# Performance work log

Measured on AMD Instinct MI355X. Metric: run time of the kernel, lower is better.

## Reference

```python
import jax, jax.numpy as jnp
import numpy as np

# Grid config from init_kwargs
VX, VY = 0.1, 0.1
XMIN, YMIN, ZMIN, XMAX, YMAX, ZMAX = 0.0, -25.6, -3.0, 51.2, 25.6, 3.0
H = int(round((XMAX - XMIN) / VX))  # 512
W = int(round((YMAX - YMIN) / VY))  # 512
SIGMA = 1.5   # gaussian std in voxel units
R = 3         # splat window radius -> 7x7 kernel


def _pose0to1(pose0, pose1):
    # ego-motion: pose1^{-1} @ pose0, per batch element
    return jnp.linalg.inv(pose1) @ pose0


def _transform(xyz, pose):
    # xyz: [B,N,3], pose: [B,4,4] -> xyz @ R^T + t
    Rm = pose[:, :3, :3]
    t = pose[:, :3, 3]
    return jnp.einsum('bnd,bed->bne', xyz, Rm) + t[:, None, :]


def _voxelize(xyz):
    # continuous voxel coords + integer pillar indices + in-range mask
    px = (xyz[..., 0] - XMIN) / VX
    py = (xyz[..., 1] - YMIN) / VY
    ix = jnp.floor(px).astype(jnp.int32)
    iy = jnp.floor(py).astype(jnp.int32)
    valid = (ix >= 0) & (ix < H) & (iy >= 0) & (iy < W) & \
            (xyz[..., 2] >= ZMIN) & (xyz[..., 2] < ZMAX)
    return px, py, ix, iy, valid


def _gauss_heatmap(px, py, ix, iy, valid):
    # Splat a gaussian (max-composited) around every valid radar pillar.
    B, M = px.shape
    offs = jnp.arange(-R, R + 1)
    dx, dy = jnp.meshgrid(offs, offs, indexing='ij')      # [K,K]
    gx = ix[:, :, None, None] + dx                        # [B,M,K,K]
    gy = iy[:, :, None, None] + dy
    cellx = gx.astype(px.dtype) + 0.5
    celly = gy.astype(py.dtype) + 0.5
    d2 = (cellx - px[:, :, None, None]) ** 2 + (celly - py[:, :, None, None]) ** 2
    val = jnp.exp(-d2 / (2.0 * SIGMA * SIGMA))
    inb = (gx >= 0) & (gx < H) & (gy >= 0) & (gy < W) & valid[:, :, None, None]
    bidx = jnp.arange(B, dtype=jnp.int32)[:, None, None, None]
    flat = jnp.where(inb, bidx * (H * W) + gx * W + gy, B * H * W)  # dummy seg for invalid
    heat = jax.ops.segment_max(val.reshape(-1), flat.reshape(-1),
                               num_segments=B * H * W + 1)
    heat = jnp.maximum(heat[:B * H * W], 0.0).reshape(B, H, W)
    return heat


def _gather(heat, ix, iy, valid):
    # per-point gaussian score = heatmap at the point's pillar
    B = heat.shape[0]
    hf = heat.reshape(B, -1)
    idx = jnp.clip(ix, 0, H - 1) * W + jnp.clip(iy, 0, W - 1)
    s = jnp.take_along_axis(hf, idx, axis=1)
    return jnp.where(valid, s, 0.0)


def _forward(pc0, pc1, radar_pc0, radar_pc1, pose0, pose1):
    # pose computed under no_grad in the original -> stop_gradient
    pose_0to1 = jax.lax.stop_gradient(_pose0to1(pose0, pose1))
    tpc0 = _transform(pc0, pose_0to1)
    trad0_xyz = _transform(radar_pc0[..., :3], pose_0to1)
    # dynamic pillar voxelization (BEV coords)
    _, _, l0x, l0y, l0v = _voxelize(tpc0)
    _, _, l1x, l1y, l1v = _voxelize(pc1)
    r0px, r0py, r0x, r0y, r0v = _voxelize(trad0_xyz)
    r1px, r1py, r1x, r1y, r1v = _voxelize(radar_pc1[..., :3])
    # gaussian maps from radar pillars, scored for lidar + radar points
    heat0 = _gauss_heatmap(r0px, r0py, r0x, r0y, r0v)
    heat1 = _gauss_heatmap(r1px, r1py, r1x, r1y, r1v)
    lidar0 = _gather(heat0, l0x, l0y, l0v)   # [B,N]
    radar0 = _gather(heat0, r0x, r0y, r0v)   # [B,M]
    lidar1 = _gather(heat1, l1x, l1y, l1v)
    radar1 = _gather(heat1, r1x, r1y, r1v)
    return jnp.concatenate([lidar0, radar0, lidar1, radar1], axis=1)


def setup_inputs() -> dict:
    key = jax.random.key(0)
    ks = jax.random.split(key, 8)
    B, N, M = 8, 262144, 8192
    lo = jnp.array([XMIN, YMIN, ZMIN], dtype=jnp.float32)
    hi = jnp.array([XMAX, YMAX, ZMAX], dtype=jnp.float32)
    pc0 = jax.random.uniform(ks[0], (B, N, 3), dtype=jnp.float32) * (hi - lo) + lo
    pc1 = jax.random.uniform(ks[1], (B, N, 3), dtype=jnp.float32) * (hi - lo) + lo
    rxyz0 = jax.random.uniform(ks[2], (B, M, 3), dtype=jnp.float32) * (hi - lo) + lo
    rxyz1 = jax.random.uniform(ks[3], (B, M, 3), dtype=jnp.float32) * (hi - lo) + lo
    radar_pc0 = jnp.concatenate([rxyz0, jax.random.normal(ks[4], (B, M, 3), dtype=jnp.float32)], axis=-1)
    radar_pc1 = jnp.concatenate([rxyz1, jax.random.normal(ks[5], (B, M, 3), dtype=jnp.float32)], axis=-1)

    def mk_pose(k):
        t = jax.random.uniform(k, (B, 3), minval=-0.5, maxval=0.5, dtype=jnp.float32)
        eye = jnp.tile(jnp.eye(4, dtype=jnp.float32)[None], (B, 1, 1))
        return eye.at[:, :3, 3].set(t)

    pose0 = mk_pose(ks[6])
    pose1 = mk_pose(ks[7])
    return {"pc0": pc0, "pc1": pc1, "radar_pc0": radar_pc0,
            "radar_pc1": radar_pc1, "pose0": pose0, "pose1": pose1}


def reference(pc0, pc1, radar_pc0, radar_pc1, pose0, pose1):
    return _forward(pc0, pc1, radar_pc0, radar_pc1, pose0, pose1)
```

## Files before the change

kernel.cpp:

```cpp
#include <hip/hip_runtime.h>
#include <math.h>

#define GH 512
#define GW 512
#define GHW (GH * GW)
#define RR 3
#define SH 16
#define SSHIFT 4
#define NSTRIP (GH / SH)
#define SCAP 1024
#define THR 1024
#define GTHR 256

typedef float f32x4 __attribute__((ext_vector_type(4)));


__device__ __forceinline__ void compute_pose(const float* __restrict__ P0,
                                             const float* __restrict__ P1,
                                             float* __restrict__ T) {
    float a00 = P1[0], a01 = P1[1], a02 = P1[2],  t1x = P1[3];
    float a10 = P1[4], a11 = P1[5], a12 = P1[6],  t1y = P1[7];
    float a20 = P1[8], a21 = P1[9], a22 = P1[10], t1z = P1[11];
    float c00 = a11 * a22 - a12 * a21;
    float c01 = a12 * a20 - a10 * a22;
    float c02 = a10 * a21 - a11 * a20;
    float det = a00 * c00 + a01 * c01 + a02 * c02;
    float id = 1.0f / det;
    float r00 = c00 * id;
    float r01 = (a02 * a21 - a01 * a22) * id;
    float r02 = (a01 * a12 - a02 * a11) * id;
    float r10 = c01 * id;
    float r11 = (a00 * a22 - a02 * a20) * id;
    float r12 = (a02 * a10 - a00 * a12) * id;
    float r20 = c02 * id;
    float r21 = (a01 * a20 - a00 * a21) * id;
    float r22 = (a00 * a11 - a01 * a10) * id;

    float b00 = P0[0], b01 = P0[1], b02 = P0[2],  t0x = P0[3];
    float b10 = P0[4], b11 = P0[5], b12 = P0[6],  t0y = P0[7];
    float b20 = P0[8], b21 = P0[9], b22 = P0[10], t0z = P0[11];
    float dx = t0x - t1x, dy = t0y - t1y, dz = t0z - t1z;

    T[0]  = r00 * b00 + r01 * b10 + r02 * b20;
    T[1]  = r00 * b01 + r01 * b11 + r02 * b21;
    T[2]  = r00 * b02 + r01 * b12 + r02 * b22;
    T[3]  = r00 * dx + r01 * dy + r02 * dz;
    T[4]  = r10 * b00 + r11 * b10 + r12 * b20;
    T[5]  = r10 * b01 + r11 * b11 + r12 * b21;
    T[6]  = r10 * b02 + r11 * b12 + r12 * b22;
    T[7]  = r10 * dx + r11 * dy + r12 * dz;
    T[8]  = r20 * b00 + r21 * b10 + r22 * b20;
    T[9]  = r20 * b01 + r21 * b11 + r22 * b21;
    T[10] = r20 * b02 + r21 * b12 + r22 * b22;
    T[11] = r20 * dx + r21 * dy + r22 * dz;
}

__device__ __forceinline__ void voxelize_xyz(float x, float y, float z,
                                             const float* __restrict__ T,
                                             float& px, float& py,
                                             int& ix, int& iy, bool& valid) {
    if (T) {
        float nx = T[0] * x + T[1] * y + T[2] * z + T[3];
        float ny = T[4] * x + T[5] * y + T[6] * z + T[7];
        float nz = T[8] * x + T[9] * y + T[10] * z + T[11];
        x = nx; y = ny; z = nz;
    }
    px = (x - 0.0f) * 10.0f;
    py = (y - (-25.6f)) * 10.0f;
    ix = (int)floorf(px);
    iy = (int)floorf(py);
    valid = (ix >= 0) & (ix < GH) & (iy >= 0) & (iy < GW) &
            (z >= -3.0f) & (z < 3.0f);
}

__global__ __launch_bounds__(THR, 8)
void heat_strip_kernel(const float* __restrict__ radar0,
                       const float* __restrict__ radar1,
                       const float* __restrict__ pose0,
                       const float* __restrict__ pose1,
                       float* __restrict__ heat0,
                       float* __restrict__ heat1,
                       int B, int M) {
    __shared__ int strip[SH * GW];
    __shared__ float2 sp[SCAP];
    __shared__ float Tsh[8][12];
    __shared__ int sn;

    const int tid = threadIdx.x;
    const int lane = tid & 63;
    const int blk = blockIdx.x;
    const int b = blk % B;
    const int map = (blk / B) & 1;
    const int sx = blk / (2 * B);
    const int x0 = sx << SSHIFT;

    if (tid < B) compute_pose(pose0 + tid * 16, pose1 + tid * 16, &Tsh[tid][0]);
    if (tid == 0) sn = 0;
    {
        const int4 z4 = make_int4(0, 0, 0, 0);
        for (int c4 = tid * 4; c4 < SH * GW; c4 += 4 * THR)
            *reinterpret_cast<int4*>(&strip[c4]) = z4;
    }
    __syncthreads();

    const float* radar = map ? radar1 : radar0;
    const float* pb = radar + (size_t)b * M * 6;
    const f32x4* pb4 = reinterpret_cast<const f32x4*>(pb);
    const bool hasT = (map == 0);
    const float* T = &Tsh[b][0];

    const int ng = M >> 2;
    for (int g0 = 0; g0 < ng; g0 += THR) {
        int g = g0 + tid;
        bool inr = (g < ng);
        float X[4], Y[4], Z[4];
        if (inr) {
            const f32x4* s = pb4 + (size_t)g * 6;
            f32x4 q0 = s[0], q1 = s[1], q2 = s[2];
            f32x4 q3 = s[3], q4 = s[4], q5 = s[5];
            X[0] = q0.x; Y[0] = q0.y; Z[0] = q0.z;
            X[1] = q1.z; Y[1] = q1.w; Z[1] = q2.x;
            X[2] = q3.x; Y[2] = q3.y; Z[2] = q3.z;
            X[3] = q4.z; Y[3] = q4.w; Z[3] = q5.x;
        }
        #pragma unroll
        for (int j = 0; j < 4; j++) {
            bool valid = false;
            float px = 0.0f, py = 0.0f;
            if (inr) {
                float x = X[j], y = Y[j], z = Z[j];
                float nx = hasT ? (T[0] * x + T[1] * y + T[2] * z + T[3]) : x;
                px = (nx - 0.0f) * 10.0f;
                int ix = (int)floorf(px);
                if (ix >= x0 - RR && ix <= x0 + SH - 1 + RR) {
                    float ny = hasT ? (T[4] * x + T[5] * y + T[6] * z + T[7]) : y;
                    float nz = hasT ? (T[8] * x + T[9] * y + T[10] * z + T[11]) : z;
                    py = (ny - (-25.6f)) * 10.0f;
                    int iy = (int)floorf(py);
                    valid = (ix >= 0) & (ix < GH) & (iy >= 0) & (iy < GW) &
                            (nz >= -3.0f) & (nz < 3.0f);
                }
            }
            unsigned long long mask = __ballot(valid);
            if (valid) {
                int leader = __ffsll((long long)mask) - 1;
                int cnt = __popcll(mask);
                int wbase = 0;
                if (lane == leader) wbase = atomicAdd(&sn, cnt);
                wbase = __shfl(wbase, leader);
                int off = __popcll(mask & ((1ull << lane) - 1ull));
                int slot = wbase + off;
                if (slot < SCAP) sp[slot] = make_float2(px, py);
            }
        }
    }
    if (M & 3) {
        int i = (M & ~3) + tid;
        bool valid = false;
        float px = 0.0f, py = 0.0f;
        if (i < M) {
            const float* p = pb + (size_t)i * 6;
            float x = p[0], y = p[1], z = p[2];
            float nx = hasT ? (T[0] * x + T[1] * y + T[2] * z + T[3]) : x;
            px = (nx - 0.0f) * 10.0f;
            int ix = (int)floorf(px);
            if (ix >= x0 - RR && ix <= x0 + SH - 1 + RR) {
                float ny = hasT ? (T[4] * x + T[5] * y + T[6] * z + T[7]) : y;
                float nz = hasT ? (T[8] * x + T[9] * y + T[10] * z + T[11]) : z;
                py = (ny - (-25.6f)) * 10.0f;
                int iy = (int)floorf(py);
                valid = (ix >= 0) & (ix < GH) & (iy >= 0) & (iy < GW) &
                        (nz >= -3.0f) & (nz < 3.0f);
            }
        }
        unsigned long long mask = __ballot(valid);
        if (valid) {
            int leader = __ffsll((long long)mask) - 1;
            int cnt = __popcll(mask);
            int wbase = 0;
            if (lane == leader) wbase = atomicAdd(&sn, cnt);
            wbase = __shfl(wbase, leader);
            int off = __popcll(mask & ((1ull << lane) - 1ull));
            int slot = wbase + off;
            if (slot < SCAP) sp[slot] = make_float2(px, py);
        }
    }
    __syncthreads();

    int n = sn; if (n > SCAP) n = SCAP;
    const int total = n * 49;
    for (int t = tid; t < total; t += THR) {
        int pi = t / 49;
        int c = t - pi * 49;
        float px = sp[pi].x;
        float py = sp[pi].y;
        int ix = (int)floorf(px);
        int iy = (int)floorf(py);
        int dx = c / 7 - RR;
        int dy = c - (c / 7) * 7 - RR;
        int gx = ix + dx, gy = iy + dy;
        if (gx < x0 || gx >= x0 + SH || gy < 0 || gy >= GW) continue;
        float ddx = ((float)gx + 0.5f) - px;
        float ddy = ((float)gy + 0.5f) - py;
        float d2 = ddx * ddx + ddy * ddy;
        float val = expf(-d2 / 4.5f);
        atomicMax(&strip[(gx - x0) * GW + gy], __float_as_int(val));
    }
    __syncthreads();

    float* heat = map ? heat1 : heat0;
    float* hb = heat + (size_t)b * GHW + (size_t)x0 * GW;
    for (int c4 = tid * 4; c4 < SH * GW; c4 += 4 * THR) {
        int4 iv = *reinterpret_cast<const int4*>(&strip[c4]);
        float4 fv;
        fv.x = __int_as_float(iv.x);
        fv.y = __int_as_float(iv.y);
        fv.z = __int_as_float(iv.z);
        fv.w = __int_as_float(iv.w);
        *reinterpret_cast<float4*>(hb + c4) = fv;
    }
}

__global__ __launch_bounds__(GTHR)
void gather_vec_kernel(const float* __restrict__ pc0,
                       const float* __restrict__ pc1,
                       const float* __restrict__ radar0,
                       const float* __restrict__ radar1,
                       const float* __restrict__ pose0,
                       const float* __restrict__ pose1,
                       const float* __restrict__ heat0,
                       const float* __restrict__ heat1,
                       float* __restrict__ out,
                       int N, int M) {
    __shared__ float Tsh[12];
    const int row_len = 2 * N + 2 * M;
    const int b = blockIdx.x;

    if (threadIdx.x == 0) compute_pose(pose0 + b * 16, pose1 + b * 16, Tsh);
    __syncthreads();

    const float* hb0 = heat0 + (size_t)b * GHW;
    const float* hb1 = heat1 + (size_t)b * GHW;

    const int ncp = N >> 10;
    const int ncr = M >> 10;
    const int c = blockIdx.y;

    const float* segbase;
    const float* T = nullptr;
    const float* hb;
    int stride, out_base, pseg;
    if (c < ncp) {
        segbase = pc0 + (size_t)b * N * 3; stride = 3;
        out_base = 0;          T = Tsh; hb = hb0; pseg = c << 10;
    } else if (c < ncp + ncr) {
        segbase = radar0 + (size_t)b * M * 6; stride = 6;
        out_base = N;          T = Tsh; hb = hb0; pseg = (c - ncp) << 10;
    } else if (c < 2 * ncp + ncr) {
        segbase = pc1 + (size_t)b * N * 3; stride = 3;
        out_base = N + M;               hb = hb1; pseg = (c - ncp - ncr) << 10;
    } else {
        segbase = radar1 + (size_t)b * M * 6; stride = 6;
        out_base = 2 * N + M;           hb = hb1; pseg = (c - 2 * ncp - ncr) << 10;
    }

    const int p0 = pseg + threadIdx.x * 4;
    float X[4], Y[4], Z[4];
    if (stride == 3) {
        const f32x4* s = reinterpret_cast<const f32x4*>(segbase + (size_t)p0 * 3);
        f32x4 f0 = __builtin_nontemporal_load(s + 0);
        f32x4 f1 = __builtin_nontemporal_load(s + 1);
        f32x4 f2 = __builtin_nontemporal_load(s + 2);
        X[0] = f0.x; Y[0] = f0.y; Z[0] = f0.z;
        X[1] = f0.w; Y[1] = f1.x; Z[1] = f1.y;
        X[2] = f1.z; Y[2] = f1.w; Z[2] = f2.x;
        X[3] = f2.y; Y[3] = f2.z; Z[3] = f2.w;
    } else {
        const f32x4* s = reinterpret_cast<const f32x4*>(segbase + (size_t)p0 * 6);
        f32x4 g0 = __builtin_nontemporal_load(s + 0);
        f32x4 g1 = __builtin_nontemporal_load(s + 1);
        f32x4 g2 = __builtin_nontemporal_load(s + 2);
        f32x4 g3 = __builtin_nontemporal_load(s + 3);
        f32x4 g4 = __builtin_nontemporal_load(s + 4);
        f32x4 g5 = __builtin_nontemporal_load(s + 5);
        X[0] = g0.x; Y[0] = g0.y; Z[0] = g0.z;
        X[1] = g1.z; Y[1] = g1.w; Z[1] = g2.x;
        X[2] = g3.x; Y[2] = g3.y; Z[2] = g3.z;
        X[3] = g4.z; Y[3] = g4.w; Z[3] = g5.x;
    }

    float v[4];
    #pragma unroll
    for (int k = 0; k < 4; k++) {
        float px, py; int ix, iy; bool valid;
        voxelize_xyz(X[k], Y[k], Z[k], T, px, py, ix, iy, valid);
        v[k] = 0.0f;
        if (valid) v[k] = hb[ix * GW + iy];
    }

    f32x4 res;
    res.x = v[0]; res.y = v[1]; res.z = v[2]; res.w = v[3];
    __builtin_nontemporal_store(res,
        reinterpret_cast<f32x4*>(out + (size_t)b * row_len + out_base + p0));
}

__global__ __launch_bounds__(GTHR)
void gather_fused_kernel(const float* __restrict__ pc0,
                         const float* __restrict__ pc1,
                         const float* __restrict__ radar0,
                         const float* __restrict__ radar1,
                         const float* __restrict__ pose0,
                         const float* __restrict__ pose1,
                         const float* __restrict__ heat0,
                         const float* __restrict__ heat1,
                         float* __restrict__ out,
                         int N, int M) {
    __shared__ float Tsh[12];
    const int row_len = 2 * N + 2 * M;
    const int b = blockIdx.x;
    const int base = blockIdx.y * 1024 + threadIdx.x;

    if (threadIdx.x == 0) compute_pose(pose0 + b * 16, pose1 + b * 16, Tsh);
    __syncthreads();

    const float* hb0 = heat0 + (size_t)b * GHW;
    const float* hb1 = heat1 + (size_t)b * GHW;

    #pragma unroll
    for (int k = 0; k < 4; k++) {
        int r = base + k * GTHR;
        if (r >= row_len) continue;
        const float* p;
        const float* T = nullptr;
        const float* hb;
        if (r < N) {
            p = pc0 + ((size_t)b * N + r) * 3; T = Tsh; hb = hb0;
        } else if (r < N + M) {
            p = radar0 + ((size_t)b * M + (r - N)) * 6; T = Tsh; hb = hb0;
        } else if (r < 2 * N + M) {
            p = pc1 + ((size_t)b * N + (r - N - M)) * 3; hb = hb1;
        } else {
            p = radar1 + ((size_t)b * M + (r - 2 * N - M)) * 6; hb = hb1;
        }
        float px, py; int ix, iy; bool valid;
        voxelize_xyz(p[0], p[1], p[2], T, px, py, ix, iy, valid);
        float v = 0.0f;
        if (valid) v = hb[ix * GW + iy];
        __builtin_nontemporal_store(v, out + (size_t)b * row_len + r);
    }
}

extern "C" void kernel_launch(void* const* d_in, const int* in_sizes, int n_in,
                              void* d_out, int out_size, void* d_ws, size_t ws_size,
                              hipStream_t stream) {
    const float* pc0      = (const float*)d_in[0];
    const float* pc1      = (const float*)d_in[1];
    const float* radar0   = (const float*)d_in[2];
    const float* radar1   = (const float*)d_in[3];
    const float* pose0    = (const float*)d_in[4];
    const float* pose1    = (const float*)d_in[5];
    float* out = (float*)d_out;

    int B = in_sizes[4] / 16;
    int N = in_sizes[0] / (B * 3);
    int M = in_sizes[2] / (B * 6);
    int row_len = 2 * N + 2 * M;

    float* heat0 = (float*)d_ws;
    float* heat1 = heat0 + (size_t)B * GHW;

    int nblk = 2 * B * NSTRIP;
    heat_strip_kernel<<<nblk, THR, 0, stream>>>(
        radar0, radar1, pose0, pose1, heat0, heat1, B, M);

    if (((N & 1023) == 0) && ((M & 1023) == 0)) {
        dim3 ggrid(B, 2 * (N >> 10) + 2 * (M >> 10));
        gather_vec_kernel<<<ggrid, GTHR, 0, stream>>>(
            pc0, pc1, radar0, radar1, pose0, pose1, heat0, heat1, out, N, M);
    } else {
        dim3 ggrid(B, (row_len + 1023) / 1024);
        gather_fused_kernel<<<ggrid, GTHR, 0, stream>>>(
            pc0, pc1, radar0, radar1, pose0, pose1, heat0, heat1, out, N, M);
    }
}
```

Baseline: 148.3 us.

## Stage gather inputs through LDS and double heat strip height

The gather kernel now copies each 1024-point chunk of the xyz input into shared memory with fully coalesced vector loads. Each thread then processes points at a stride of one block width, so the scalar output stores and heatmap reads are coalesced across lanes. Radar rows are read whole, including the unused 3 channels, which the old per-thread load also did. Separately, the heat strip height goes from 16 to 32 rows (halving the strip block count and doubling the strip LDS buffer) and the occupancy hint is dropped from the launch bounds.

After: 140.0 us. -5.6%, faster.

```diff
diff --git a/kernel.cpp b/kernel.cpp
--- a/kernel.cpp
+++ b/kernel.cpp
@@ -5,12 +5,13 @@
 #define GW 512
 #define GHW (GH * GW)
 #define RR 3
-#define SH 16
-#define SSHIFT 4
+#define SH 32
+#define SSHIFT 5
 #define NSTRIP (GH / SH)
 #define SCAP 1024
 #define THR 1024
 #define GTHR 256
+#define GCH 1024
 
 typedef float f32x4 __attribute__((ext_vector_type(4)));
 
@@ -73,7 +74,7 @@
             (z >= -3.0f) & (z < 3.0f);
 }
 
-__global__ __launch_bounds__(THR, 8)
+__global__ __launch_bounds__(THR)
 void heat_strip_kernel(const float* __restrict__ radar0,
                        const float* __restrict__ radar1,
                        const float* __restrict__ pose0,
@@ -222,7 +223,7 @@
 }
 
 __global__ __launch_bounds__(GTHR)
-void gather_vec_kernel(const float* __restrict__ pc0,
+void gather_lds_kernel(const float* __restrict__ pc0,
                        const float* __restrict__ pc1,
                        const float* __restrict__ radar0,
                        const float* __restrict__ radar1,
@@ -232,18 +233,16 @@
                        const float* __restrict__ heat1,
                        float* __restrict__ out,
                        int N, int M) {
+    __shared__ float stage[6 * GCH];
     __shared__ float Tsh[12];
+    const int tid = threadIdx.x;
     const int row_len = 2 * N + 2 * M;
     const int b = blockIdx.x;
 
-    if (threadIdx.x == 0) compute_pose(pose0 + b * 16, pose1 + b * 16, Tsh);
-    __syncthreads();
-
-    const float* hb0 = heat0 + (size_t)b * GHW;
-    const float* hb1 = heat1 + (size_t)b * GHW;
-
-    const int ncp = N >> 10;
-    const int ncr = M >> 10;
+    if (tid == 0) compute_pose(pose0 + b * 16, pose1 + b * 16, Tsh);
+
+    const int ncp = N / GCH;
+    const int ncr = M / GCH;
     const int c = blockIdx.y;
 
     const float* segbase;
@@ -252,56 +251,40 @@
     int stride, out_base, pseg;
     if (c < ncp) {
         segbase = pc0 + (size_t)b * N * 3; stride = 3;
-        out_base = 0;          T = Tsh; hb = hb0; pseg = c << 10;
+        out_base = 0;          T = Tsh; hb = heat0; pseg = c * GCH;
     } else if (c < ncp + ncr) {
         segbase = radar0 + (size_t)b * M * 6; stride = 6;
-        out_base = N;          T = Tsh; hb = hb0; pseg = (c - ncp) << 10;
+        out_base = N;          T = Tsh; hb = heat0; pseg = (c - ncp) * GCH;
     } else if (c < 2 * ncp + ncr) {
         segbase = pc1 + (size_t)b * N * 3; stride = 3;
-        out_base = N + M;               hb = hb1; pseg = (c - ncp - ncr) << 10;
+        out_base = N + M;               hb = heat1; pseg = (c - ncp - ncr) * GCH;
     } else {
         segbase = radar1 + (size_t)b * M * 6; stride = 6;
-        out_base = 2 * N + M;           hb = hb1; pseg = (c - 2 * ncp - ncr) << 10;
-    }
-
-    const int p0 = pseg + threadIdx.x * 4;
-    float X[4], Y[4], Z[4];
-    if (stride == 3) {
-        const f32x4* s = reinterpret_cast<const f32x4*>(segbase + (size_t)p0 * 3);
-        f32x4 f0 = __builtin_nontemporal_load(s + 0);
-        f32x4 f1 = __builtin_nontemporal_load(s + 1);
-        f32x4 f2 = __builtin_nontemporal_load(s + 2);
-        X[0] = f0.x; Y[0] = f0.y; Z[0] = f0.z;
-        X[1] = f0.w; Y[1] = f1.x; Z[1] = f1.y;
-        X[2] = f1.z; Y[2] = f1.w; Z[2] = f2.x;
-        X[3] = f2.y; Y[3] = f2.z; Z[3] = f2.w;
-    } else {
-        const f32x4* s = reinterpret_cast<const f32x4*>(segbase + (size_t)p0 * 6);
-        f32x4 g0 = __builtin_nontemporal_load(s + 0);
-        f32x4 g1 = __builtin_nontemporal_load(s + 1);
-        f32x4 g2 = __builtin_nontemporal_load(s + 2);
-        f32x4 g3 = __builtin_nontemporal_load(s + 3);
-        f32x4 g4 = __builtin_nontemporal_load(s + 4);
-        f32x4 g5 = __builtin_nontemporal_load(s + 5);
-        X[0] = g0.x; Y[0] = g0.y; Z[0] = g0.z;
-        X[1] = g1.z; Y[1] = g1.w; Z[1] = g2.x;
-        X[2] = g3.x; Y[2] = g3.y; Z[2] = g3.z;
-        X[3] = g4.z; Y[3] = g4.w; Z[3] = g5.x;
-    }
-
-    float v[4];
+        out_base = 2 * N + M;           hb = heat1; pseg = (c - 2 * ncp - ncr) * GCH;
+    }
+    const float* hbb = hb + (size_t)b * GHW;
+
+    {
+        const f32x4* src = reinterpret_cast<const f32x4*>(
+            segbase + (size_t)pseg * stride);
+        f32x4* dst = reinterpret_cast<f32x4*>(stage);
+        const int nv = (GCH * stride) >> 2;
+        for (int i = tid; i < nv; i += GTHR)
+            dst[i] = __builtin_nontemporal_load(src + i);
+    }
+    __syncthreads();
+
+    float* ob = out + (size_t)b * row_len + out_base + pseg;
     #pragma unroll
-    for (int k = 0; k < 4; k++) {
+    for (int j = 0; j < GCH / GTHR; j++) {
+        int k = j * GTHR + tid;
+        const float* p = stage + k * stride;
         float px, py; int ix, iy; bool valid;
-        voxelize_xyz(X[k], Y[k], Z[k], T, px, py, ix, iy, valid);
-        v[k] = 0.0f;
-        if (valid) v[k] = hb[ix * GW + iy];
-    }
-
-    f32x4 res;
-    res.x = v[0]; res.y = v[1]; res.z = v[2]; res.w = v[3];
-    __builtin_nontemporal_store(res,
-        reinterpret_cast<f32x4*>(out + (size_t)b * row_len + out_base + p0));
+        voxelize_xyz(p[0], p[1], p[2], T, px, py, ix, iy, valid);
+        float v = 0.0f;
+        if (valid) v = hbb[ix * GW + iy];
+        __builtin_nontemporal_store(v, ob + k);
+    }
 }
 
 __global__ __launch_bounds__(GTHR)
@@ -373,9 +356,9 @@
     heat_strip_kernel<<<nblk, THR, 0, stream>>>(
         radar0, radar1, pose0, pose1, heat0, heat1, B, M);
 
-    if (((N & 1023) == 0) && ((M & 1023) == 0)) {
-        dim3 ggrid(B, 2 * (N >> 10) + 2 * (M >> 10));
-        gather_vec_kernel<<<ggrid, GTHR, 0, stream>>>(
+    if ((N % GCH) == 0 && (M % GCH) == 0) {
+        dim3 ggrid(B, 2 * (N / GCH) + 2 * (M / GCH));
+        gather_lds_kernel<<<ggrid, GTHR, 0, stream>>>(
             pc0, pc1, radar0, radar1, pose0, pose1, heat0, heat1, out, N, M);
     } else {
         dim3 ggrid(B, (row_len + 1023) / 1024);
```
